# Performance work log

Measured on AMD Instinct MI355X. Metric: run time of the kernel, lower is better.

## Reference

```python
import jax, jax.numpy as jnp
import numpy as np
from jax import lax

B, T, D, H, L = 64, 1024, 256, 1024, 2


def setup_inputs() -> dict:
    key = jax.random.key(0)
    ks = jax.random.split(key, 9)
    s = 0.03  # small init so tanh/sigmoid stay in sane range
    return {
        "x": jax.random.normal(ks[0], (B, T, D), dtype=jnp.float32),
        "W_ih0": jax.random.normal(ks[1], (4 * H, D), dtype=jnp.float32) * s,
        "W_hh0": jax.random.normal(ks[2], (4 * H, H), dtype=jnp.float32) * s,
        "b_ih0": jax.random.normal(ks[3], (4 * H,), dtype=jnp.float32) * s,
        "b_hh0": jax.random.normal(ks[4], (4 * H,), dtype=jnp.float32) * s,
        "W_ih1": jax.random.normal(ks[5], (4 * H, H), dtype=jnp.float32) * s,
        "W_hh1": jax.random.normal(ks[6], (4 * H, H), dtype=jnp.float32) * s,
        "b_ih1": jax.random.normal(ks[7], (4 * H,), dtype=jnp.float32) * s,
        "b_hh1": jax.random.normal(ks[8], (4 * H,), dtype=jnp.float32) * s,
    }


def _lstm_layer(x, W_ih, W_hh, b_ih, b_hh):
    """Single LSTM layer over full sequence. x: [B,T,Din]. Returns (ys [B,T,H], h [B,H], c [B,H])."""
    b, t = x.shape[0], x.shape[1]
    h_dim = W_hh.shape[1]
    # Precompute input projections for all timesteps in one GEMM.
    xg = jnp.einsum('bti,gi->btg', x, W_ih) + b_ih + b_hh  # [B,T,4H]

    def step(carry, xg_t):
        h, c = carry
        g = xg_t + h @ W_hh.T  # [B,4H]
        i, f, gg, o = jnp.split(g, 4, axis=-1)  # PyTorch gate order i,f,g,o
        i = jax.nn.sigmoid(i)
        f = jax.nn.sigmoid(f)
        gg = jnp.tanh(gg)
        o = jax.nn.sigmoid(o)
        c = f * c + i * gg
        h = o * jnp.tanh(c)
        return (h, c), h

    h0 = jnp.zeros((b, h_dim), x.dtype)
    (h, c), ys = lax.scan(step, (h0, h0), jnp.swapaxes(xg, 0, 1))
    return jnp.swapaxes(ys, 0, 1), h, c


def reference(x, W_ih0, W_hh0, b_ih0, b_hh0, W_ih1, W_hh1, b_ih1, b_hh1):
    # Dropout layers are identity in eval mode; nn.LSTM inter-layer dropout
    # is also inactive in eval, so the math is a plain stacked LSTM whose
    # final (h, c) per layer is returned, matching the torch forward().
    y0, h0_, c0_ = _lstm_layer(x, W_ih0, W_hh0, b_ih0, b_hh0)
    _, h1_, c1_ = _lstm_layer(y0, W_ih1, W_hh1, b_ih1, b_hh1)
    h = jnp.stack([h0_, h1_], axis=0)  # [L,B,H]
    c = jnp.stack([c0_, c1_], axis=0)  # [L,B,H]
    return (h, c)
```

## Files before the change

kernel.cpp:

```cpp
#include <hip/hip_runtime.h>

#define NWG     256
#define TPB     256
#define NL0     128
#define T_STEPS 1024
#define HD      1024
#define DIN     256
#define K0      1280
#define K1      2048
#define K0P     1288
#define K1P     2056
#define SMEM_BYTES (32*K1P*2)

#define HSLAB_BYTES 131072ull
#define HSLAB_U64   16384
#define HIST_DEPTH  1025
#define HIST_BYTES  (HIST_DEPTH*HSLAB_BYTES)
#define X8_BYTES    33554432ull
#define FLAGS_BYTES 32768ull
#define NGEN        16

typedef float  f32x4  __attribute__((ext_vector_type(4)));
typedef __bf16 bf16x8 __attribute__((ext_vector_type(8)));
typedef unsigned long long u64;

__device__ __forceinline__ unsigned short f2bf(float f){
  union { float f; unsigned u; } a; a.f = f;
  unsigned u = a.u;
  u += 0x7fffu + ((u >> 16) & 1u);
  return (unsigned short)(u >> 16);
}
__device__ __forceinline__ float sigmf(float x){ return 1.0f/(1.0f + __expf(-x)); }
__device__ __forceinline__ float tanhf_fast(float x){ return 2.0f*sigmf(2.0f*x) - 1.0f; }

__device__ __forceinline__ u64 ld64c(const u64* p){
  return __hip_atomic_load(p, __ATOMIC_RELAXED, __HIP_MEMORY_SCOPE_AGENT);
}
__device__ __forceinline__ void st16c(unsigned short* p, unsigned short v){
  __hip_atomic_store(p, v, __ATOMIC_RELAXED, __HIP_MEMORY_SCOPE_AGENT);
}
__device__ __forceinline__ unsigned ldflag(const unsigned* p){
  return __hip_atomic_load(p, __ATOMIC_RELAXED, __HIP_MEMORY_SCOPE_AGENT);
}
__device__ __forceinline__ void stflag(unsigned* p, unsigned v){
  __hip_atomic_store(p, v, __ATOMIC_RELAXED, __HIP_MEMORY_SCOPE_AGENT);
}

__device__ __forceinline__ void gridbar(unsigned* flags, unsigned ep, int wg, int tid){
  asm volatile("s_waitcnt vmcnt(0)" ::: "memory");
  __syncthreads();
  if (tid == 0) stflag(&flags[wg*16], ep);
  while (ldflag(&flags[tid*16]) < ep) __builtin_amdgcn_s_sleep(1);
  __syncthreads();
}

__global__ void xpose_kernel(const float* __restrict__ x, unsigned short* __restrict__ X8){
  int idx   = blockIdx.x*256 + threadIdx.x;
  int t     = idx >> 11;
  int rem   = idx & 2047;
  int plane = rem >> 6;
  int b     = rem & 63;
  const float* src = x + ((size_t)b << 18) + (t << 8) + (plane << 3);
  unsigned short tmp[8];
  #pragma unroll
  for (int j = 0; j < 8; ++j) tmp[j] = f2bf(src[j]);
  int4 v; __builtin_memcpy(&v, tmp, 16);
  ((int4*)X8)[idx] = v;
}

template<bool H0C, bool H1C>
__global__ void __launch_bounds__(TPB, 1)
lstm_mega(const float* __restrict__ Wih0, const float* __restrict__ Whh0,
          const float* __restrict__ bih0, const float* __restrict__ bhh0,
          const float* __restrict__ Wih1, const float* __restrict__ Whh1,
          const float* __restrict__ bih1, const float* __restrict__ bhh1,
          const unsigned short* __restrict__ X8,
          unsigned* flags, unsigned* gen,
          u64* H0, u64* H1, int d0, int d1,
          float* __restrict__ out)
{
  extern __shared__ unsigned short Ws[];
  const int tid   = threadIdx.x;
  const int wg    = blockIdx.x;
  const int layer = (wg >= NL0);
  const int wgl   = layer ? wg - NL0 : wg;
  const int KD    = layer ? K1  : K0;
  const int dlen  = layer ? HD  : DIN;
  const int KP    = layer ? K1P : K0P;
  const int4* X4  = (const int4*)X8;

  {
    const float* Wih = layer ? Wih1 : Wih0;
    const float* Whh = layer ? Whh1 : Whh0;
    for (int m = 0; m < 32; ++m){
      int gr = (m & 3)*HD + wgl*8 + (m >> 2);
      const float* ar = Wih + (size_t)gr*dlen;
      const float* br = Whh + (size_t)gr*HD;
      unsigned short* row = Ws + m*KP;
      for (int k = tid; k < KD; k += TPB)
        row[k] = f2bf(k < dlen ? ar[k] : br[k - dlen]);
    }
  }
  __syncthreads();

  const int lane  = tid & 63;
  const int wv    = tid >> 6;
  const int q     = lane >> 4;
  const int nn    = lane & 15;
  const int batch = wv*16 + nn;

  float bias[2][4];
  {
    const float* bi = layer ? bih1 : bih0;
    const float* bh = layer ? bhh1 : bhh0;
    #pragma unroll
    for (int rt = 0; rt < 2; ++rt){
      int colr = wgl*8 + rt*4 + q;
      #pragma unroll
      for (int r = 0; r < 4; ++r)
        bias[rt][r] = bi[r*HD + colr] + bh[r*HD + colr];
    }
  }

  float cst[2] = {0.f, 0.f};
  float hv[2]  = {0.f, 0.f};

  auto do_step = [&](int t){
    f32x4 a00 = {0,0,0,0}, a01 = {0,0,0,0}, a10 = {0,0,0,0}, a11 = {0,0,0,0};

    auto MM = [&](int kb, bf16x8 b){
      bf16x8 a0, a1;
      __builtin_memcpy(&a0, &Ws[nn*KP + kb*32 + q*8], 16);
      __builtin_memcpy(&a1, &Ws[(16+nn)*KP + kb*32 + q*8], 16);
      if (kb & 1){ a01 = __builtin_amdgcn_mfma_f32_16x16x32_bf16(a0,b,a01,0,0,0);
                   a11 = __builtin_amdgcn_mfma_f32_16x16x32_bf16(a1,b,a11,0,0,0); }
      else       { a00 = __builtin_amdgcn_mfma_f32_16x16x32_bf16(a0,b,a00,0,0,0);
                   a10 = __builtin_amdgcn_mfma_f32_16x16x32_bf16(a1,b,a10,0,0,0); }
    };

    if (!layer){
      const int4* xb = X4 + (size_t)t*2048;
      const u64* hb  = H0 + (size_t)(t % d0)*HSLAB_U64;

      int4 xr[8];
      #pragma unroll
      for (int kb = 0; kb < 8; ++kb)
        xr[kb] = xb[(kb*4 + q)*64 + batch];

      u64 B[3][16];
      auto LD = [&](int c){
        u64* d = B[c % 3];
        #pragma unroll
        for (int i = 0; i < 8; ++i){
          const u64* p = hb + (((c*8 + i)*4 + q)*64 + batch)*2;
          d[2*i]   = H0C ? ld64c(p)     : p[0];
          d[2*i+1] = H0C ? ld64c(p + 1) : p[1];
        }
      };
      LD(0); LD(1);
      #pragma unroll
      for (int kb = 0; kb < 8; ++kb){
        bf16x8 b; __builtin_memcpy(&b, &xr[kb], 16);
        MM(kb, b);
      }
      LD(2);
      #pragma unroll
      for (int c = 0; c < 4; ++c){
        u64* d = B[c % 3];
        #pragma unroll
        for (int i = 0; i < 8; ++i){
          u64 pair[2] = {d[2*i], d[2*i+1]};
          bf16x8 b; __builtin_memcpy(&b, pair, 16);
          MM(8 + c*8 + i, b);
        }
        if (c + 3 < 4) LD(c + 3);
      }
    } else {
      const u64* yb = H0 + (size_t)((t+1) % d0)*HSLAB_U64;
      const u64* hb = H1 + (size_t)(t % d1)*HSLAB_U64;

      u64 B[3][16];
      auto LD = [&](int c){
        const u64* src = (c < 4) ? yb : hb;
        int p0 = (c & 3)*8;
        u64* d = B[c % 3];
        #pragma unroll
        for (int i = 0; i < 8; ++i){
          const u64* p = src + (((p0 + i)*4 + q)*64 + batch)*2;
          if (c < 4){ d[2*i] = H0C ? ld64c(p) : p[0];
                      d[2*i+1] = H0C ? ld64c(p + 1) : p[1]; }
          else      { d[2*i] = H1C ? ld64c(p) : p[0];
                      d[2*i+1] = H1C ? ld64c(p + 1) : p[1]; }
        }
      };
      LD(0); LD(1); LD(2);
      #pragma unroll
      for (int c = 0; c < 8; ++c){
        u64* d = B[c % 3];
        #pragma unroll
        for (int i = 0; i < 8; ++i){
          u64 pair[2] = {d[2*i], d[2*i+1]};
          bf16x8 b; __builtin_memcpy(&b, pair, 16);
          MM(c*8 + i, b);
        }
        if (c + 3 < 8) LD(c + 3);
      }
    }

    f32x4 s0 = a00 + a01, s1 = a10 + a11;
    u64* Hw = layer ? H1 : H0;
    int  wd = layer ? d1 : d0;
    unsigned short* wbase = (unsigned short*)(Hw + (size_t)((t+1) % wd)*HSLAB_U64);
    #pragma unroll
    for (int rt = 0; rt < 2; ++rt){
      f32x4 s = rt ? s1 : s0;
      float ii = sigmf(s[0] + bias[rt][0]);
      float ff = sigmf(s[1] + bias[rt][1]);
      float gg = tanhf_fast(s[2] + bias[rt][2]);
      float oo = sigmf(s[3] + bias[rt][3]);
      cst[rt] = ff*cst[rt] + ii*gg;
      hv[rt]  = oo*tanhf_fast(cst[rt]);
      st16c(wbase + (wgl*64 + batch)*8 + (rt*4 + q), f2bf(hv[rt]));
    }
  };

  if (!layer){
    for (int s = 0; s < T_STEPS; ++s){
      do_step(s);
      gridbar(flags, (unsigned)(s+1), wg, tid);
    }
  } else {
    for (int s = 0; s < T_STEPS; ++s){
      if (s > 0) do_step(s-1);
      gridbar(flags, (unsigned)(s+1), wg, tid);
    }
    do_step(T_STEPS-1);
  }

  {
    int col0 = wgl*8 + q;
    int base = layer ? 65536 : 0;
    out[base          + batch*HD + col0    ] = hv[0];
    out[base          + batch*HD + col0 + 4] = hv[1];
    out[base + 131072 + batch*HD + col0    ] = cst[0];
    out[base + 131072 + batch*HD + col0 + 4] = cst[1];
  }
}

extern "C" void kernel_launch(void* const* d_in, const int* in_sizes, int n_in,
                              void* d_out, int out_size, void* d_ws, size_t ws_size,
                              hipStream_t stream)
{
  const float* x    = (const float*)d_in[0];
  const float* Wih0 = (const float*)d_in[1];
  const float* Whh0 = (const float*)d_in[2];
  const float* bih0 = (const float*)d_in[3];
  const float* bhh0 = (const float*)d_in[4];
  const float* Wih1 = (const float*)d_in[5];
  const float* Whh1 = (const float*)d_in[6];
  const float* bih1 = (const float*)d_in[7];
  const float* bhh1 = (const float*)d_in[8];
  float* out = (float*)d_out;

  char* ws = (char*)d_ws;
  unsigned* flags = (unsigned*)ws;
  unsigned* gen   = (unsigned*)(ws + 16384);

  const size_t need2 = FLAGS_BYTES + 2*HIST_BYTES + X8_BYTES;
  const size_t need1 = FLAGS_BYTES + HIST_BYTES + 2*HSLAB_BYTES + X8_BYTES;

  u64 *H0p, *H1p; unsigned short* X8p; int d0, d1, tier;
  if (ws_size >= need2){
    tier = 2; d0 = HIST_DEPTH; d1 = HIST_DEPTH;
    H0p = (u64*)(ws + FLAGS_BYTES);
    H1p = (u64*)(ws + FLAGS_BYTES + HIST_BYTES);
    X8p = (unsigned short*)(ws + FLAGS_BYTES + 2*HIST_BYTES);
  } else if (ws_size >= need1){
    tier = 1; d0 = HIST_DEPTH; d1 = 2;
    H0p = (u64*)(ws + FLAGS_BYTES);
    H1p = (u64*)(ws + FLAGS_BYTES + HIST_BYTES);
    X8p = (unsigned short*)(ws + FLAGS_BYTES + HIST_BYTES + 2*HSLAB_BYTES);
  } else {
    tier = 0; d0 = 2; d1 = 2;
    H0p = (u64*)(ws + FLAGS_BYTES);
    H1p = (u64*)(ws + FLAGS_BYTES + 2*HSLAB_BYTES);
    X8p = (unsigned short*)(ws + FLAGS_BYTES + 4*HSLAB_BYTES);
  }

  hipMemsetAsync(flags, 0, FLAGS_BYTES, stream);
  hipMemsetAsync(H0p, 0, HSLAB_BYTES, stream);
  hipMemsetAsync(H1p, 0, HSLAB_BYTES, stream);
  xpose_kernel<<<8192, 256, 0, stream>>>(x, X8p);

  void* fn = (tier == 2) ? (void*)&lstm_mega<false,false>
           : (tier == 1) ? (void*)&lstm_mega<false,true>
                         : (void*)&lstm_mega<true,true>;
  hipFuncSetAttribute(fn, hipFuncAttributeMaxDynamicSharedMemorySize, SMEM_BYTES);

  const unsigned short* X8c = X8p;
  void* args[] = {(void*)&Wih0,(void*)&Whh0,(void*)&bih0,(void*)&bhh0,
                  (void*)&Wih1,(void*)&Whh1,(void*)&bih1,(void*)&bhh1,
                  (void*)&X8c,(void*)&flags,(void*)&gen,
                  (void*)&H0p,(void*)&H1p,(void*)&d0,(void*)&d1,(void*)&out};
  hipError_t err = hipLaunchCooperativeKernel(fn, dim3(NWG), dim3(TPB),
                                              args, SMEM_BYTES, stream);
  if (err != hipSuccess){
    if (tier == 2)
      lstm_mega<false,false><<<dim3(NWG), dim3(TPB), SMEM_BYTES, stream>>>(
        Wih0,Whh0,bih0,bhh0,Wih1,Whh1,bih1,bhh1,X8c,flags,gen,H0p,H1p,d0,d1,out);
    else if (tier == 1)
      lstm_mega<false,true><<<dim3(NWG), dim3(TPB), SMEM_BYTES, stream>>>(
        Wih0,Whh0,bih0,bhh0,Wih1,Whh1,bih1,bhh1,X8c,flags,gen,H0p,H1p,d0,d1,out);
    else
      lstm_mega<true,true><<<dim3(NWG), dim3(TPB), SMEM_BYTES, stream>>>(
        Wih0,Whh0,bih0,bhh0,Wih1,Whh1,bih1,bhh1,X8c,flags,gen,H0p,H1p,d0,d1,out);
  }
}
```

Measured before the change: 6.457 ms.

## Split K across wave pairs with LDS reduction, vectorized h stores, decoupled layer-0 barrier

Each wave pair now splits the reduction dimension in half and covers 32 batches with two B fragments. This reuses each LDS weight fragment across two MFMAs, and partial sums are reduced through a small LDS buffer. Hidden-state writes are packed via shuffles into single 128-bit coherent stores instead of many 16-bit atomics. Layer-0 workgroups poll only layer-0 flags when the history buffer is deep enough, so they can run ahead of layer 1. The cost is an extra __syncthreads and an LDS round-trip per step, plus higher register pressure from larger prefetch buffers.

```diff
diff --git a/kernel.cpp b/kernel.cpp
--- a/kernel.cpp
+++ b/kernel.cpp
@@ -10,7 +10,8 @@
 #define K1      2048
 #define K0P     1288
 #define K1P     2056
-#define SMEM_BYTES (32*K1P*2)
+#define REDSZ   8192
+#define SMEM_BYTES (32*K1P*2 + REDSZ)
 
 #define HSLAB_BYTES 131072ull
 #define HSLAB_U64   16384
@@ -18,10 +19,10 @@
 #define HIST_BYTES  (HIST_DEPTH*HSLAB_BYTES)
 #define X8_BYTES    33554432ull
 #define FLAGS_BYTES 32768ull
-#define NGEN        16
 
 typedef float  f32x4  __attribute__((ext_vector_type(4)));
 typedef __bf16 bf16x8 __attribute__((ext_vector_type(8)));
+typedef int    i32x4  __attribute__((ext_vector_type(4)));
 typedef unsigned long long u64;
 
 __device__ __forceinline__ unsigned short f2bf(float f){
@@ -36,21 +37,35 @@
 __device__ __forceinline__ u64 ld64c(const u64* p){
   return __hip_atomic_load(p, __ATOMIC_RELAXED, __HIP_MEMORY_SCOPE_AGENT);
 }
-__device__ __forceinline__ void st16c(unsigned short* p, unsigned short v){
-  __hip_atomic_store(p, v, __ATOMIC_RELAXED, __HIP_MEMORY_SCOPE_AGENT);
-}
 __device__ __forceinline__ unsigned ldflag(const unsigned* p){
   return __hip_atomic_load(p, __ATOMIC_RELAXED, __HIP_MEMORY_SCOPE_AGENT);
 }
 __device__ __forceinline__ void stflag(unsigned* p, unsigned v){
   __hip_atomic_store(p, v, __ATOMIC_RELAXED, __HIP_MEMORY_SCOPE_AGENT);
 }
-
-__device__ __forceinline__ void gridbar(unsigned* flags, unsigned ep, int wg, int tid){
+__device__ __forceinline__ void st128c(void* p, i32x4 v){
+  asm volatile("global_store_dwordx4 %0, %1, off sc0 sc1" :: "v"(p), "v"(v) : "memory");
+}
+__device__ __forceinline__ i32x4 ld128(const void* p, bool coh){
+  if (coh){
+    u64 a = ld64c((const u64*)p);
+    u64 b = ld64c(((const u64*)p) + 1);
+    i32x4 r;
+    __builtin_memcpy(&r, &a, 8);
+    __builtin_memcpy(((char*)&r) + 8, &b, 8);
+    return r;
+  }
+  i32x4 r;
+  __builtin_memcpy(&r, p, 16);
+  return r;
+}
+
+__device__ __forceinline__ void gridbar(unsigned* flags, unsigned ep, int wg, int tid, int npoll){
   asm volatile("s_waitcnt vmcnt(0)" ::: "memory");
   __syncthreads();
   if (tid == 0) stflag(&flags[wg*16], ep);
-  while (ldflag(&flags[tid*16]) < ep) __builtin_amdgcn_s_sleep(1);
+  if (tid < npoll)
+    while (ldflag(&flags[tid*16]) < ep) __builtin_amdgcn_s_sleep(1);
   __syncthreads();
 }
 
@@ -87,7 +102,7 @@
   const int KD    = layer ? K1  : K0;
   const int dlen  = layer ? HD  : DIN;
   const int KP    = layer ? K1P : K0P;
-  const int4* X4  = (const int4*)X8;
+  const char* X8b = (const char*)X8;
 
   {
     const float* Wih = layer ? Wih1 : Wih0;
@@ -107,110 +122,37 @@
   const int wv    = tid >> 6;
   const int q     = lane >> 4;
   const int nn    = lane & 15;
-  const int batch = wv*16 + nn;
+  const int bh    = wv >> 1;
+  const int kh    = wv & 1;
+  const int batA  = bh*32 + nn;
+  const int batB  = bh*32 + 16 + nn;
+
+  f32x4* Red = (f32x4*)(Ws + 32*KP);
 
   float bias[2][4];
   {
-    const float* bi = layer ? bih1 : bih0;
-    const float* bh = layer ? bhh1 : bhh0;
+    const float* bi  = layer ? bih1 : bih0;
+    const float* bhp = layer ? bhh1 : bhh0;
     #pragma unroll
     for (int rt = 0; rt < 2; ++rt){
       int colr = wgl*8 + rt*4 + q;
       #pragma unroll
       for (int r = 0; r < 4; ++r)
-        bias[rt][r] = bi[r*HD + colr] + bh[r*HD + colr];
+        bias[rt][r] = bi[r*HD + colr] + bhp[r*HD + colr];
     }
   }
 
   float cst[2] = {0.f, 0.f};
   float hv[2]  = {0.f, 0.f};
 
-  auto do_step = [&](int t){
-    f32x4 a00 = {0,0,0,0}, a01 = {0,0,0,0}, a10 = {0,0,0,0}, a11 = {0,0,0,0};
-
-    auto MM = [&](int kb, bf16x8 b){
-      bf16x8 a0, a1;
-      __builtin_memcpy(&a0, &Ws[nn*KP + kb*32 + q*8], 16);
-      __builtin_memcpy(&a1, &Ws[(16+nn)*KP + kb*32 + q*8], 16);
-      if (kb & 1){ a01 = __builtin_amdgcn_mfma_f32_16x16x32_bf16(a0,b,a01,0,0,0);
-                   a11 = __builtin_amdgcn_mfma_f32_16x16x32_bf16(a1,b,a11,0,0,0); }
-      else       { a00 = __builtin_amdgcn_mfma_f32_16x16x32_bf16(a0,b,a00,0,0,0);
-                   a10 = __builtin_amdgcn_mfma_f32_16x16x32_bf16(a1,b,a10,0,0,0); }
-    };
-
-    if (!layer){
-      const int4* xb = X4 + (size_t)t*2048;
-      const u64* hb  = H0 + (size_t)(t % d0)*HSLAB_U64;
-
-      int4 xr[8];
-      #pragma unroll
-      for (int kb = 0; kb < 8; ++kb)
-        xr[kb] = xb[(kb*4 + q)*64 + batch];
-
-      u64 B[3][16];
-      auto LD = [&](int c){
-        u64* d = B[c % 3];
-        #pragma unroll
-        for (int i = 0; i < 8; ++i){
-          const u64* p = hb + (((c*8 + i)*4 + q)*64 + batch)*2;
-          d[2*i]   = H0C ? ld64c(p)     : p[0];
-          d[2*i+1] = H0C ? ld64c(p + 1) : p[1];
-        }
-      };
-      LD(0); LD(1);
-      #pragma unroll
-      for (int kb = 0; kb < 8; ++kb){
-        bf16x8 b; __builtin_memcpy(&b, &xr[kb], 16);
-        MM(kb, b);
-      }
-      LD(2);
-      #pragma unroll
-      for (int c = 0; c < 4; ++c){
-        u64* d = B[c % 3];
-        #pragma unroll
-        for (int i = 0; i < 8; ++i){
-          u64 pair[2] = {d[2*i], d[2*i+1]};
-          bf16x8 b; __builtin_memcpy(&b, pair, 16);
-          MM(8 + c*8 + i, b);
-        }
-        if (c + 3 < 4) LD(c + 3);
-      }
-    } else {
-      const u64* yb = H0 + (size_t)((t+1) % d0)*HSLAB_U64;
-      const u64* hb = H1 + (size_t)(t % d1)*HSLAB_U64;
-
-      u64 B[3][16];
-      auto LD = [&](int c){
-        const u64* src = (c < 4) ? yb : hb;
-        int p0 = (c & 3)*8;
-        u64* d = B[c % 3];
-        #pragma unroll
-        for (int i = 0; i < 8; ++i){
-          const u64* p = src + (((p0 + i)*4 + q)*64 + batch)*2;
-          if (c < 4){ d[2*i] = H0C ? ld64c(p) : p[0];
-                      d[2*i+1] = H0C ? ld64c(p + 1) : p[1]; }
-          else      { d[2*i] = H1C ? ld64c(p) : p[0];
-                      d[2*i+1] = H1C ? ld64c(p + 1) : p[1]; }
-        }
-      };
-      LD(0); LD(1); LD(2);
-      #pragma unroll
-      for (int c = 0; c < 8; ++c){
-        u64* d = B[c % 3];
-        #pragma unroll
-        for (int i = 0; i < 8; ++i){
-          u64 pair[2] = {d[2*i], d[2*i+1]};
-          bf16x8 b; __builtin_memcpy(&b, pair, 16);
-          MM(c*8 + i, b);
-        }
-        if (c + 3 < 8) LD(c + 3);
-      }
-    }
-
-    f32x4 s0 = a00 + a01, s1 = a10 + a11;
-    u64* Hw = layer ? H1 : H0;
-    int  wd = layer ? d1 : d0;
-    unsigned short* wbase = (unsigned short*)(Hw + (size_t)((t+1) % wd)*HSLAB_U64);
+  auto epilogue = [&](f32x4 a00, f32x4 a01, f32x4 a10, f32x4 a11,
+                      u64* Hw, int wd, int t){
+    Red[(wv*2+0)*64 + lane] = kh ? a00 : a01;
+    Red[(wv*2+1)*64 + lane] = kh ? a10 : a11;
+    __syncthreads();
+    const int pw = wv ^ 1;
+    f32x4 s0 = (kh ? a01 : a00) + Red[(pw*2+0)*64 + lane];
+    f32x4 s1 = (kh ? a11 : a10) + Red[(pw*2+1)*64 + lane];
     #pragma unroll
     for (int rt = 0; rt < 2; ++rt){
       f32x4 s = rt ? s1 : s0;
@@ -220,26 +162,111 @@
       float oo = sigmf(s[3] + bias[rt][3]);
       cst[rt] = ff*cst[rt] + ii*gg;
       hv[rt]  = oo*tanhf_fast(cst[rt]);
-      st16c(wbase + (wgl*64 + batch)*8 + (rt*4 + q), f2bf(hv[rt]));
+    }
+    unsigned hpk = ((unsigned)f2bf(hv[1]) << 16) | (unsigned)f2bf(hv[0]);
+    unsigned g0 = __shfl(hpk, nn);
+    unsigned g1 = __shfl(hpk, nn + 16);
+    unsigned g2 = __shfl(hpk, nn + 32);
+    unsigned g3 = __shfl(hpk, nn + 48);
+    if (q == 0){
+      i32x4 v;
+      v.x = (int)((g0 & 0xffffu) | (g1 << 16));
+      v.y = (int)((g2 & 0xffffu) | (g3 << 16));
+      v.z = (int)((g0 >> 16) | (g1 & 0xffff0000u));
+      v.w = (int)((g2 >> 16) | (g3 & 0xffff0000u));
+      char* wbase = (char*)(Hw + (size_t)((t+1) % wd)*HSLAB_U64);
+      st128c(wbase + ((wgl*64 + wv*16 + nn) << 4), v);
     }
   };
 
+  auto step0 = [&](int t){
+    const char* hb0 = (const char*)(H0 + (size_t)(t % d0)*HSLAB_U64);
+    const char* xb  = X8b + ((size_t)t << 15);
+    i32x4 Bf[40];
+    #pragma unroll
+    for (int j = 0; j < 20; ++j){
+      const int kb = kh*20 + j;
+      if (kb < 8){
+        const char* p = xb + (((kb*4 + q)*64) << 4);
+        Bf[2*j]   = ld128(p + (batA << 4), false);
+        Bf[2*j+1] = ld128(p + (batB << 4), false);
+      } else {
+        const char* p = hb0 + ((((kb-8)*4 + q)*64) << 4);
+        Bf[2*j]   = ld128(p + (batA << 4), H0C);
+        Bf[2*j+1] = ld128(p + (batB << 4), H0C);
+      }
+    }
+    f32x4 a00 = {0,0,0,0}, a01 = {0,0,0,0}, a10 = {0,0,0,0}, a11 = {0,0,0,0};
+    #pragma unroll
+    for (int j = 0; j < 20; ++j){
+      const int kb = kh*20 + j;
+      bf16x8 a0, a1, v0, v1;
+      __builtin_memcpy(&a0, &Ws[nn*KP + kb*32 + q*8], 16);
+      __builtin_memcpy(&a1, &Ws[(16+nn)*KP + kb*32 + q*8], 16);
+      __builtin_memcpy(&v0, &Bf[2*j], 16);
+      __builtin_memcpy(&v1, &Bf[2*j+1], 16);
+      a00 = __builtin_amdgcn_mfma_f32_16x16x32_bf16(a0, v0, a00, 0, 0, 0);
+      a01 = __builtin_amdgcn_mfma_f32_16x16x32_bf16(a0, v1, a01, 0, 0, 0);
+      a10 = __builtin_amdgcn_mfma_f32_16x16x32_bf16(a1, v0, a10, 0, 0, 0);
+      a11 = __builtin_amdgcn_mfma_f32_16x16x32_bf16(a1, v1, a11, 0, 0, 0);
+    }
+    epilogue(a00, a01, a10, a11, H0, d0, t);
+  };
+
+  auto step1 = [&](int t){
+    const char* yb  = (const char*)(H0 + (size_t)((t+1) % d0)*HSLAB_U64);
+    const char* hb1 = (const char*)(H1 + (size_t)(t % d1)*HSLAB_U64);
+    const char* src = kh ? hb1 : yb;
+    const bool  coh = kh ? H1C : H0C;
+    i32x4 Bf[6][8];
+    auto LDC = [&](int c){
+      const int g   = c >> 1;
+      const int bat = (c & 1) ? batB : batA;
+      const char* p = src + (((g*32 + q)*64 + bat) << 4);
+      #pragma unroll
+      for (int i = 0; i < 8; ++i)
+        Bf[c % 6][i] = ld128(p + i*4096, coh);
+    };
+    LDC(0); LDC(1); LDC(2); LDC(3); LDC(4); LDC(5);
+    f32x4 a00 = {0,0,0,0}, a01 = {0,0,0,0}, a10 = {0,0,0,0}, a11 = {0,0,0,0};
+    #pragma unroll
+    for (int g = 0; g < 4; ++g){
+      #pragma unroll
+      for (int i = 0; i < 8; ++i){
+        const int kb = kh*32 + g*8 + i;
+        bf16x8 a0, a1, v0, v1;
+        __builtin_memcpy(&a0, &Ws[nn*KP + kb*32 + q*8], 16);
+        __builtin_memcpy(&a1, &Ws[(16+nn)*KP + kb*32 + q*8], 16);
+        __builtin_memcpy(&v0, &Bf[(2*g) % 6][i], 16);
+        __builtin_memcpy(&v1, &Bf[(2*g+1) % 6][i], 16);
+        a00 = __builtin_amdgcn_mfma_f32_16x16x32_bf16(a0, v0, a00, 0, 0, 0);
+        a01 = __builtin_amdgcn_mfma_f32_16x16x32_bf16(a0, v1, a01, 0, 0, 0);
+        a10 = __builtin_amdgcn_mfma_f32_16x16x32_bf16(a1, v0, a10, 0, 0, 0);
+        a11 = __builtin_amdgcn_mfma_f32_16x16x32_bf16(a1, v1, a11, 0, 0, 0);
+      }
+      if (g == 0){ LDC(6); LDC(7); }
+    }
+    epilogue(a00, a01, a10, a11, H1, d1, t);
+  };
+
   if (!layer){
+    const int npoll0 = (d0 >= T_STEPS + 1) ? NL0 : NWG;
     for (int s = 0; s < T_STEPS; ++s){
-      do_step(s);
-      gridbar(flags, (unsigned)(s+1), wg, tid);
+      step0(s);
+      gridbar(flags, (unsigned)(s+1), wg, tid, npoll0);
     }
   } else {
     for (int s = 0; s < T_STEPS; ++s){
-      if (s > 0) do_step(s-1);
-      gridbar(flags, (unsigned)(s+1), wg, tid);
-    }
-    do_step(T_STEPS-1);
+      if (s > 0) step1(s-1);
+      gridbar(flags, (unsigned)(s+1), wg, tid, NWG);
+    }
+    step1(T_STEPS-1);
   }
 
   {
-    int col0 = wgl*8 + q;
-    int base = layer ? 65536 : 0;
+    const int col0  = wgl*8 + q;
+    const int base  = layer ? 65536 : 0;
+    const int batch = wv*16 + nn;
     out[base          + batch*HD + col0    ] = hv[0];
     out[base          + batch*HD + col0 + 4] = hv[1];
     out[base + 131072 + batch*HD + col0    ] = cst[0];
```

Result: slower. 7.527 ms (+16.6%).

## Decouple LSTM layers with per-layer flag waits and packed 128-bit h stores

Applied to the files above, without the earlier changes.

Replaces the full grid barrier after every timestep with split waits. Layer-0 workgroups wait only on layer-0 flags. Layer-1 waits on layer-0's step t+1 flag before loading y, and on layer-1 flags only before loading its own h. The waits are placed after some MFMA work, which overlaps flag polling with computation. When the history buffer is deep enough, this lets the layers run as a pipeline instead of in lockstep. The per-element 16-bit h stores are also replaced with lane shuffles and a single 128-bit coherent store per 16 lanes. The cost is more complex synchronization logic that depends on the history buffer depth and inline asm cache bits.

```diff
diff --git a/kernel.cpp b/kernel.cpp
--- a/kernel.cpp
+++ b/kernel.cpp
@@ -18,10 +18,10 @@
 #define HIST_BYTES  (HIST_DEPTH*HSLAB_BYTES)
 #define X8_BYTES    33554432ull
 #define FLAGS_BYTES 32768ull
-#define NGEN        16
 
 typedef float  f32x4  __attribute__((ext_vector_type(4)));
 typedef __bf16 bf16x8 __attribute__((ext_vector_type(8)));
+typedef int    i32x4  __attribute__((ext_vector_type(4)));
 typedef unsigned long long u64;
 
 __device__ __forceinline__ unsigned short f2bf(float f){
@@ -36,22 +36,14 @@
 __device__ __forceinline__ u64 ld64c(const u64* p){
   return __hip_atomic_load(p, __ATOMIC_RELAXED, __HIP_MEMORY_SCOPE_AGENT);
 }
-__device__ __forceinline__ void st16c(unsigned short* p, unsigned short v){
-  __hip_atomic_store(p, v, __ATOMIC_RELAXED, __HIP_MEMORY_SCOPE_AGENT);
-}
 __device__ __forceinline__ unsigned ldflag(const unsigned* p){
   return __hip_atomic_load(p, __ATOMIC_RELAXED, __HIP_MEMORY_SCOPE_AGENT);
 }
 __device__ __forceinline__ void stflag(unsigned* p, unsigned v){
   __hip_atomic_store(p, v, __ATOMIC_RELAXED, __HIP_MEMORY_SCOPE_AGENT);
 }
-
-__device__ __forceinline__ void gridbar(unsigned* flags, unsigned ep, int wg, int tid){
-  asm volatile("s_waitcnt vmcnt(0)" ::: "memory");
-  __syncthreads();
-  if (tid == 0) stflag(&flags[wg*16], ep);
-  while (ldflag(&flags[tid*16]) < ep) __builtin_amdgcn_s_sleep(1);
-  __syncthreads();
+__device__ __forceinline__ void st128c(void* p, i32x4 v){
+  asm volatile("global_store_dwordx4 %0, %1, off sc0 sc1" :: "v"(p), "v"(v) : "memory");
 }
 
 __global__ void xpose_kernel(const float* __restrict__ x, unsigned short* __restrict__ X8){
@@ -124,93 +116,59 @@
 
   float cst[2] = {0.f, 0.f};
   float hv[2]  = {0.f, 0.f};
-
-  auto do_step = [&](int t){
-    f32x4 a00 = {0,0,0,0}, a01 = {0,0,0,0}, a10 = {0,0,0,0}, a11 = {0,0,0,0};
-
-    auto MM = [&](int kb, bf16x8 b){
-      bf16x8 a0, a1;
-      __builtin_memcpy(&a0, &Ws[nn*KP + kb*32 + q*8], 16);
-      __builtin_memcpy(&a1, &Ws[(16+nn)*KP + kb*32 + q*8], 16);
-      if (kb & 1){ a01 = __builtin_amdgcn_mfma_f32_16x16x32_bf16(a0,b,a01,0,0,0);
-                   a11 = __builtin_amdgcn_mfma_f32_16x16x32_bf16(a1,b,a11,0,0,0); }
-      else       { a00 = __builtin_amdgcn_mfma_f32_16x16x32_bf16(a0,b,a00,0,0,0);
-                   a10 = __builtin_amdgcn_mfma_f32_16x16x32_bf16(a1,b,a10,0,0,0); }
-    };
-
-    if (!layer){
-      const int4* xb = X4 + (size_t)t*2048;
-      const u64* hb  = H0 + (size_t)(t % d0)*HSLAB_U64;
-
-      int4 xr[8];
-      #pragma unroll
-      for (int kb = 0; kb < 8; ++kb)
-        xr[kb] = xb[(kb*4 + q)*64 + batch];
-
-      u64 B[3][16];
-      auto LD = [&](int c){
-        u64* d = B[c % 3];
-        #pragma unroll
-        for (int i = 0; i < 8; ++i){
-          const u64* p = hb + (((c*8 + i)*4 + q)*64 + batch)*2;
-          d[2*i]   = H0C ? ld64c(p)     : p[0];
-          d[2*i+1] = H0C ? ld64c(p + 1) : p[1];
-        }
-      };
-      LD(0); LD(1);
-      #pragma unroll
-      for (int kb = 0; kb < 8; ++kb){
-        bf16x8 b; __builtin_memcpy(&b, &xr[kb], 16);
-        MM(kb, b);
-      }
-      LD(2);
-      #pragma unroll
-      for (int c = 0; c < 4; ++c){
-        u64* d = B[c % 3];
-        #pragma unroll
-        for (int i = 0; i < 8; ++i){
-          u64 pair[2] = {d[2*i], d[2*i+1]};
-          bf16x8 b; __builtin_memcpy(&b, pair, 16);
-          MM(8 + c*8 + i, b);
-        }
-        if (c + 3 < 4) LD(c + 3);
-      }
-    } else {
-      const u64* yb = H0 + (size_t)((t+1) % d0)*HSLAB_U64;
-      const u64* hb = H1 + (size_t)(t % d1)*HSLAB_U64;
-
-      u64 B[3][16];
-      auto LD = [&](int c){
-        const u64* src = (c < 4) ? yb : hb;
-        int p0 = (c & 3)*8;
-        u64* d = B[c % 3];
-        #pragma unroll
-        for (int i = 0; i < 8; ++i){
-          const u64* p = src + (((p0 + i)*4 + q)*64 + batch)*2;
-          if (c < 4){ d[2*i] = H0C ? ld64c(p) : p[0];
-                      d[2*i+1] = H0C ? ld64c(p + 1) : p[1]; }
-          else      { d[2*i] = H1C ? ld64c(p) : p[0];
-                      d[2*i+1] = H1C ? ld64c(p + 1) : p[1]; }
-        }
-      };
-      LD(0); LD(1); LD(2);
-      #pragma unroll
-      for (int c = 0; c < 8; ++c){
-        u64* d = B[c % 3];
-        #pragma unroll
-        for (int i = 0; i < 8; ++i){
-          u64 pair[2] = {d[2*i], d[2*i+1]};
-          bf16x8 b; __builtin_memcpy(&b, pair, 16);
-          MM(c*8 + i, b);
-        }
-        if (c + 3 < 8) LD(c + 3);
-      }
-    }
-
+  f32x4 a00, a01, a10, a11;
+
+  auto MM = [&](int kb, bf16x8 b){
+    bf16x8 a0, a1;
+    __builtin_memcpy(&a0, &Ws[nn*KP + kb*32 + q*8], 16);
+    __builtin_memcpy(&a1, &Ws[(16+nn)*KP + kb*32 + q*8], 16);
+    if (kb & 1){ a01 = __builtin_amdgcn_mfma_f32_16x16x32_bf16(a0,b,a01,0,0,0);
+                 a11 = __builtin_amdgcn_mfma_f32_16x16x32_bf16(a1,b,a11,0,0,0); }
+    else       { a00 = __builtin_amdgcn_mfma_f32_16x16x32_bf16(a0,b,a00,0,0,0);
+                 a10 = __builtin_amdgcn_mfma_f32_16x16x32_bf16(a1,b,a10,0,0,0); }
+  };
+  auto CHUNK = [&](int kb0, u64* d){
+    #pragma unroll
+    for (int i = 0; i < 8; ++i){
+      u64 pair[2] = {d[2*i], d[2*i+1]};
+      bf16x8 b; __builtin_memcpy(&b, pair, 16);
+      MM(kb0 + i, b);
+    }
+  };
+
+  unsigned seenA = 0, seenB = 0;
+  auto waitL0 = [&](unsigned ep){
+    if (tid < NL0 && seenA < ep){
+      const unsigned* p = &flags[tid*16];
+      unsigned v = ldflag(p);
+      while (v < ep){ __builtin_amdgcn_s_sleep(1); v = ldflag(p); }
+      seenA = v;
+    }
+    __syncthreads();
+  };
+  auto waitL1 = [&](unsigned ep){
+    if (tid < NL0 && seenB < ep){
+      const unsigned* p = &flags[(NL0 + tid)*16];
+      unsigned v = ldflag(p);
+      while (v < ep){ __builtin_amdgcn_s_sleep(1); v = ldflag(p); }
+      seenB = v;
+    }
+    __syncthreads();
+  };
+  auto postF = [&](unsigned ep){
+    asm volatile("s_waitcnt vmcnt(0)" ::: "memory");
+    __syncthreads();
+    if (tid == 0) stflag(&flags[wg*16], ep);
+  };
+  auto waitAll = [&](unsigned ep){
+    while (ldflag(&flags[tid*16]) < ep) __builtin_amdgcn_s_sleep(1);
+    __syncthreads();
+  };
+
+  u64 B0[16], B1[16], B2[16];
+
+  auto epilogue = [&](u64* Hw, int wd, int t){
     f32x4 s0 = a00 + a01, s1 = a10 + a11;
-    u64* Hw = layer ? H1 : H0;
-    int  wd = layer ? d1 : d0;
-    unsigned short* wbase = (unsigned short*)(Hw + (size_t)((t+1) % wd)*HSLAB_U64);
     #pragma unroll
     for (int rt = 0; rt < 2; ++rt){
       f32x4 s = rt ? s1 : s0;
@@ -220,21 +178,110 @@
       float oo = sigmf(s[3] + bias[rt][3]);
       cst[rt] = ff*cst[rt] + ii*gg;
       hv[rt]  = oo*tanhf_fast(cst[rt]);
-      st16c(wbase + (wgl*64 + batch)*8 + (rt*4 + q), f2bf(hv[rt]));
-    }
-  };
-
+    }
+    unsigned hpk = ((unsigned)f2bf(hv[1]) << 16) | (unsigned)f2bf(hv[0]);
+    unsigned g0 = __shfl(hpk, nn);
+    unsigned g1 = __shfl(hpk, nn + 16);
+    unsigned g2 = __shfl(hpk, nn + 32);
+    unsigned g3 = __shfl(hpk, nn + 48);
+    if (q == 0){
+      i32x4 v;
+      v.x = (int)((g0 & 0xffffu) | (g1 << 16));
+      v.y = (int)((g2 & 0xffffu) | (g3 << 16));
+      v.z = (int)((g0 >> 16) | (g1 & 0xffff0000u));
+      v.w = (int)((g2 >> 16) | (g3 & 0xffff0000u));
+      char* wbase = (char*)(Hw + (size_t)((t+1) % wd)*HSLAB_U64);
+      st128c(wbase + ((wgl*64 + wv*16 + nn) << 4), v);
+    }
+  };
+
+  auto step0 = [&](int t, bool dec){
+    a00 = (f32x4){0,0,0,0}; a01 = a00; a10 = a00; a11 = a00;
+    const int4* xb = X4 + (size_t)t*2048;
+    const u64* hb  = H0 + (size_t)(t % d0)*HSLAB_U64;
+    auto LDH = [&](int c, u64* d){
+      #pragma unroll
+      for (int i = 0; i < 8; ++i){
+        const u64* p = hb + (((c*8 + i)*4 + q)*64 + batch)*2;
+        d[2*i]   = H0C ? ld64c(p)     : p[0];
+        d[2*i+1] = H0C ? ld64c(p + 1) : p[1];
+      }
+    };
+    int4 xr[8];
+    #pragma unroll
+    for (int kb = 0; kb < 8; ++kb)
+      xr[kb] = xb[(kb*4 + q)*64 + batch];
+    #pragma unroll
+    for (int kb = 0; kb < 6; ++kb){
+      bf16x8 b; __builtin_memcpy(&b, &xr[kb], 16); MM(kb, b);
+    }
+    if (dec) waitL0((unsigned)t);
+    LDH(0, B0); LDH(1, B1); LDH(2, B2);
+    { bf16x8 b; __builtin_memcpy(&b, &xr[6], 16); MM(6, b);
+                __builtin_memcpy(&b, &xr[7], 16); MM(7, b); }
+    CHUNK(8,  B0); LDH(3, B0);
+    CHUNK(16, B1);
+    CHUNK(24, B2);
+    CHUNK(32, B0);
+    epilogue(H0, d0, t);
+  };
+
+  auto step1 = [&](int t, bool dec){
+    a00 = (f32x4){0,0,0,0}; a01 = a00; a10 = a00; a11 = a00;
+    const u64* yb = H0 + (size_t)((t+1) % d0)*HSLAB_U64;
+    const u64* hb = H1 + (size_t)(t % d1)*HSLAB_U64;
+    auto LDY = [&](int c, u64* d){
+      #pragma unroll
+      for (int i = 0; i < 8; ++i){
+        const u64* p = yb + (((c*8 + i)*4 + q)*64 + batch)*2;
+        d[2*i]   = H0C ? ld64c(p)     : p[0];
+        d[2*i+1] = H0C ? ld64c(p + 1) : p[1];
+      }
+    };
+    auto LDH = [&](int c, u64* d){
+      #pragma unroll
+      for (int i = 0; i < 8; ++i){
+        const u64* p = hb + (((c*8 + i)*4 + q)*64 + batch)*2;
+        d[2*i]   = H1C ? ld64c(p)     : p[0];
+        d[2*i+1] = H1C ? ld64c(p + 1) : p[1];
+      }
+    };
+    if (dec) waitL0((unsigned)(t+1));
+    LDY(0, B0); LDY(1, B1); LDY(2, B2);
+    CHUNK(0,  B0); LDY(3, B0);
+    CHUNK(8,  B1);
+    CHUNK(16, B2);
+    if (dec) waitL1((unsigned)t);
+    LDH(0, B1); LDH(1, B2);
+    CHUNK(24, B0);
+    LDH(2, B0);
+    CHUNK(32, B1);
+    LDH(3, B1);
+    CHUNK(40, B2);
+    CHUNK(48, B0);
+    CHUNK(56, B1);
+    epilogue(H1, d1, t);
+  };
+
+  const bool dec = (d0 >= T_STEPS + 1);
   if (!layer){
-    for (int s = 0; s < T_STEPS; ++s){
-      do_step(s);
-      gridbar(flags, (unsigned)(s+1), wg, tid);
+    if (dec){
+      for (int s = 0; s < T_STEPS; ++s){ step0(s, true); postF((unsigned)(s+1)); }
+    } else {
+      for (int s = 0; s < T_STEPS; ++s){
+        step0(s, false); postF((unsigned)(s+1)); waitAll((unsigned)(s+1));
+      }
     }
   } else {
-    for (int s = 0; s < T_STEPS; ++s){
-      if (s > 0) do_step(s-1);
-      gridbar(flags, (unsigned)(s+1), wg, tid);
-    }
-    do_step(T_STEPS-1);
+    if (dec){
+      for (int t = 0; t < T_STEPS; ++t){ step1(t, true); postF((unsigned)(t+1)); }
+    } else {
+      for (int s = 0; s < T_STEPS; ++s){
+        if (s > 0) step1(s-1, false);
+        postF((unsigned)(s+1)); waitAll((unsigned)(s+1));
+      }
+      step1(T_STEPS-1, false);
+    }
   }
 
   {
```

After: 5.933 ms. 8.1% less time.
